# Performance work log

Hardware: AMD Instinct MI355X
Metric: run time of the kernel (lower is better)

## Reference

```python
import jax, jax.numpy as jnp
import numpy as np

LN_EPS = 1e-5
SA_EPS = 1e-8
NUM_ITERS = 3

def layer_norm(x, w, b):
    mu = jnp.mean(x, axis=-1, keepdims=True)
    var = jnp.mean((x - mu) ** 2, axis=-1, keepdims=True)
    return (x - mu) / jnp.sqrt(var + LN_EPS) * w + b


def setup_inputs() -> dict:
    key = jax.random.key(0)
    ks = jax.random.split(key, 24)
    B, C, H, W = 128, 256, 32, 32
    D, S, MH, NC = 64, 8, 128, 15
    s = lambda k, shape, scale=0.02: jax.random.normal(k, shape, dtype=jnp.float32) * scale
    inp = {
        "x1": jax.random.normal(ks[0], (B, C, H, W), dtype=jnp.float32),
        "x2": jax.random.normal(ks[1], (B, C, H, W), dtype=jnp.float32),
        # 1x1 convs stored as [out,in]
        "conv1_w": s(ks[2], (D, C)), "conv1_b": jnp.zeros((D,), jnp.float32),
        "conv2_w": s(ks[3], (D, C)), "conv2_b": jnp.zeros((D,), jnp.float32),
        "norm_w": jnp.ones((D,), jnp.float32), "norm_b": jnp.zeros((D,), jnp.float32),
        "ni_w": jnp.ones((D,), jnp.float32), "ni_b": jnp.zeros((D,), jnp.float32),
        "ns_w": jnp.ones((D,), jnp.float32), "ns_b": jnp.zeros((D,), jnp.float32),
        "nm_w": jnp.ones((D,), jnp.float32), "nm_b": jnp.zeros((D,), jnp.float32),
        "slots_mu": s(ks[4], (1, 1, D), 1.0), "slots_log_sigma": s(ks[5], (1, 1, D), 0.1),
        "Wq": s(ks[6], (D, D), 0.1), "Wk": s(ks[7], (D, D), 0.1), "Wv": s(ks[8], (D, D), 0.1),
        "gru_wih": s(ks[9], (3 * D, D), 0.1), "gru_whh": s(ks[10], (3 * D, D), 0.1),
        "gru_bih": jnp.zeros((3 * D,), jnp.float32), "gru_bhh": jnp.zeros((3 * D,), jnp.float32),
        "mlp_w1": s(ks[11], (MH, D), 0.1), "mlp_b1": jnp.zeros((MH,), jnp.float32),
        "mlp_w2": s(ks[12], (D, MH), 0.1), "mlp_b2": jnp.zeros((D,), jnp.float32),
        "head_w": s(ks[13], (NC, D), 0.1), "head_b": jnp.zeros((NC,), jnp.float32),
        "noise": jax.random.normal(ks[14], (B, S, D), dtype=jnp.float32),
    }
    return inp


def _forward(x1, x2, conv1_w, conv1_b, conv2_w, conv2_b, norm_w, norm_b,
             ni_w, ni_b, ns_w, ns_b, nm_w, nm_b, slots_mu, slots_log_sigma,
             Wq, Wk, Wv, gru_wih, gru_whh, gru_bih, gru_bhh,
             mlp_w1, mlp_b1, mlp_w2, mlp_b2, head_w, head_b, noise):
    B = x1.shape[0]
    D = Wq.shape[0]
    # 1x1 convs then flatten to tokens: [B, H*W, D]
    t1 = jnp.einsum('bchw,dc->bhwd', x1, conv1_w).reshape(B, -1, D) + conv1_b
    t2 = jnp.einsum('bchw,dc->bhwd', x2, conv2_w).reshape(B, -1, D) + conv2_b
    inputs = jnp.concatenate([t1, t2], axis=1)          # [B, N, D]
    inputs = layer_norm(inputs, norm_w, norm_b)

    # SlotAttention
    inputs = layer_norm(inputs, ni_w, ni_b)
    k = inputs @ Wk.T                                    # [B, N, D]
    v = inputs @ Wv.T
    slots = slots_mu + jnp.exp(slots_log_sigma) * noise  # [B, S, D]
    scale = D ** -0.5
    for _ in range(NUM_ITERS):
        slots_prev = slots
        sn = layer_norm(slots, ns_w, ns_b)
        q = (sn @ Wq.T) * scale                          # [B, S, D]
        attn_logits = jnp.einsum('bnd,bsd->bns', k, q)   # [B, N, S]
        attn = jax.nn.softmax(attn_logits, axis=-1) + SA_EPS
        attn = attn / jnp.sum(attn, axis=-2, keepdims=True)
        updates = jnp.einsum('bns,bnd->bsd', attn, v)    # [B, S, D]
        # GRUCell (torch gate order: r, z, n)
        gi = updates @ gru_wih.T + gru_bih               # [B, S, 3D]
        gh = slots_prev @ gru_whh.T + gru_bhh
        ir, iz, inn = jnp.split(gi, 3, axis=-1)
        hr, hz, hn = jnp.split(gh, 3, axis=-1)
        r = jax.nn.sigmoid(ir + hr)
        z = jax.nn.sigmoid(iz + hz)
        n = jnp.tanh(inn + r * hn)
        slots = (1.0 - z) * n + z * slots_prev
        # residual MLP
        h = layer_norm(slots, nm_w, nm_b)
        h = jax.nn.relu(h @ mlp_w1.T + mlp_b1) @ mlp_w2.T + mlp_b2
        slots = slots + h

    fused = jnp.mean(slots, axis=1)                      # [B, D]
    return fused @ head_w.T + head_b                     # [B, n_classes]


def reference(x1, x2, conv1_w, conv1_b, conv2_w, conv2_b, norm_w, norm_b,
              ni_w, ni_b, ns_w, ns_b, nm_w, nm_b, slots_mu, slots_log_sigma,
              Wq, Wk, Wv, gru_wih, gru_whh, gru_bih, gru_bhh,
              mlp_w1, mlp_b1, mlp_w2, mlp_b2, head_w, head_b, noise):
    return _forward(x1, x2, conv1_w, conv1_b, conv2_w, conv2_b, norm_w, norm_b,
                    ni_w, ni_b, ns_w, ns_b, nm_w, nm_b, slots_mu, slots_log_sigma,
                    Wq, Wk, Wv, gru_wih, gru_whh, gru_bih, gru_bhh,
                    mlp_w1, mlp_b1, mlp_w2, mlp_b2, head_w, head_b, noise)
```

## Files before the change

kernel.cpp:

```cpp
#include <hip/hip_runtime.h>
#include <stdint.h>


typedef __bf16 bf16;
typedef __bf16 bf16x8 __attribute__((ext_vector_type(8)));
typedef float  f32x4  __attribute__((ext_vector_type(4)));

#define MFMA16(a, b, c) __builtin_amdgcn_mfma_f32_16x16x32_bf16((a), (b), (c), 0, 0, 0)

__global__ __launch_bounds__(256) void k0_convert(
    const float* __restrict__ c1w, const float* __restrict__ c2w,
    const float* __restrict__ wk,  const float* __restrict__ wvv,
    bf16* __restrict__ wconv, bf16* __restrict__ wkv)
{
  const int i = blockIdx.x * 256 + threadIdx.x;
  if (i < 16384) {
    wconv[i]         = (bf16)c1w[i];
    wconv[16384 + i] = (bf16)c2w[i];
  }
  if (i < 4096) {
    wkv[i]        = (bf16)wk[i];
    wkv[4096 + i] = (bf16)wvv[i];
  }
}

__global__ __launch_bounds__(256) void k1_conv_kv(
    const float* __restrict__ x1, const float* __restrict__ x2,
    const float* __restrict__ c1b, const float* __restrict__ c2b,
    const float* __restrict__ nw,  const float* __restrict__ nb,
    const float* __restrict__ niw, const float* __restrict__ nib,
    const bf16* __restrict__ wconv, const bf16* __restrict__ wkv,
    bf16* __restrict__ kbuf, bf16* __restrict__ vT)
{
  __shared__ union {
    struct { float T[64][65]; bf16 tok[64][72]; } p2;
    struct { float Tk[64][65]; float Tv[64][65]; } kv;
  } U;

  const int bx   = blockIdx.x;
  const int tile = bx & 15;
  const int img  = (bx >> 4) & 1;
  const int b    = bx >> 5;
  const int tid  = threadIdx.x;
  const int lane = tid & 63;
  const int wvid = tid >> 6;
  const int l15  = lane & 15;
  const int quad = lane >> 4;

  const float* xp = (img ? x2 : x1) + (size_t)b * (256 * 1024) + tile * 64;
  const bf16* wc  = wconv + img * (64 * 256);
  const int p     = wvid * 16 + l15;
  const float* xcol = xp + p + (size_t)quad * 8 * 1024;

  float xv[64];
  #pragma unroll
  for (int g = 0; g < 8; ++g)
    #pragma unroll
    for (int j = 0; j < 8; ++j)
      xv[g * 8 + j] = xcol[(size_t)(g * 32 + j) * 1024];

  f32x4 acc[4] = {{0.f,0.f,0.f,0.f},{0.f,0.f,0.f,0.f},{0.f,0.f,0.f,0.f},{0.f,0.f,0.f,0.f}};

  #pragma unroll
  for (int g = 0; g < 8; ++g) {
    bf16x8 af;
    #pragma unroll
    for (int j = 0; j < 8; ++j)
      af[j] = (bf16)xv[g * 8 + j];
    #pragma unroll
    for (int nt = 0; nt < 4; ++nt) {
      const bf16x8 bw = *(const bf16x8*)&wc[(nt * 16 + l15) * 256 + g * 32 + quad * 8];
      acc[nt] = MFMA16(af, bw, acc[nt]);
    }
  }

  {
    const float* cb = img ? c2b : c1b;
    #pragma unroll
    for (int nt = 0; nt < 4; ++nt) {
      const int d = nt * 16 + l15;
      const float bias = cb[d];
      #pragma unroll
      for (int r = 0; r < 4; ++r)
        U.p2.T[wvid * 16 + quad * 4 + r][d] = acc[nt][r] + bias;
    }
  }
  __syncthreads();

  {
    const int pix = tid >> 2, part = tid & 3;
    float xv2[16], yv[16];
    float s = 0.f, s2 = 0.f;
    #pragma unroll
    for (int i = 0; i < 16; ++i) {
      xv2[i] = U.p2.T[pix][part * 16 + i];
      s += xv2[i]; s2 += xv2[i] * xv2[i];
    }
    s  += __shfl_xor(s, 1);  s  += __shfl_xor(s, 2);
    s2 += __shfl_xor(s2, 1); s2 += __shfl_xor(s2, 2);
    float mu   = s * 0.015625f;
    float rstd = rsqrtf(s2 * 0.015625f - mu * mu + 1e-5f);
    s = 0.f; s2 = 0.f;
    #pragma unroll
    for (int i = 0; i < 16; ++i) {
      const int d = part * 16 + i;
      const float y = (xv2[i] - mu) * rstd * nw[d] + nb[d];
      yv[i] = y; s += y; s2 += y * y;
    }
    s  += __shfl_xor(s, 1);  s  += __shfl_xor(s, 2);
    s2 += __shfl_xor(s2, 1); s2 += __shfl_xor(s2, 2);
    mu   = s * 0.015625f;
    rstd = rsqrtf(s2 * 0.015625f - mu * mu + 1e-5f);
    #pragma unroll
    for (int i = 0; i < 16; ++i) {
      const int d = part * 16 + i;
      U.p2.tok[pix][d] = (bf16)((yv[i] - mu) * rstd * niw[d] + nib[d]);
    }
  }
  __syncthreads();

  f32x4 ak[4] = {{0.f,0.f,0.f,0.f},{0.f,0.f,0.f,0.f},{0.f,0.f,0.f,0.f},{0.f,0.f,0.f,0.f}};
  f32x4 av[4] = {{0.f,0.f,0.f,0.f},{0.f,0.f,0.f,0.f},{0.f,0.f,0.f,0.f},{0.f,0.f,0.f,0.f}};
  #pragma unroll
  for (int k0 = 0; k0 < 64; k0 += 32) {
    const bf16x8 af = *(const bf16x8*)&U.p2.tok[wvid * 16 + l15][k0 + quad * 8];
    #pragma unroll
    for (int nt = 0; nt < 4; ++nt) {
      const bf16x8 bk = *(const bf16x8*)&wkv[(nt * 16 + l15) * 64 + k0 + quad * 8];
      const bf16x8 bv = *(const bf16x8*)&wkv[4096 + (nt * 16 + l15) * 64 + k0 + quad * 8];
      ak[nt] = MFMA16(af, bk, ak[nt]);
      av[nt] = MFMA16(af, bv, av[nt]);
    }
  }
  __syncthreads();

  #pragma unroll
  for (int nt = 0; nt < 4; ++nt)
    #pragma unroll
    for (int r = 0; r < 4; ++r) {
      U.kv.Tk[wvid * 16 + quad * 4 + r][nt * 16 + l15] = ak[nt][r];
      U.kv.Tv[nt * 16 + l15][wvid * 16 + quad * 4 + r] = av[nt][r];
    }
  __syncthreads();
  {
    const int row = tid >> 2, dd = (tid & 3) * 16;
    const size_t kb = ((size_t)b * 2048 + img * 1024 + tile * 64) * 64;
    bf16 tb[16];
    #pragma unroll
    for (int i = 0; i < 16; ++i) tb[i] = (bf16)U.kv.Tk[row][dd + i];
    *(bf16x8*)&kbuf[kb + (size_t)row * 64 + dd]     = *(bf16x8*)&tb[0];
    *(bf16x8*)&kbuf[kb + (size_t)row * 64 + dd + 8] = *(bf16x8*)&tb[8];
    #pragma unroll
    for (int i = 0; i < 16; ++i) tb[i] = (bf16)U.kv.Tv[row][dd + i];
    const size_t vb = ((size_t)b * 64 + row) * 2048 + img * 1024 + tile * 64 + dd;
    *(bf16x8*)&vT[vb]     = *(bf16x8*)&tb[0];
    *(bf16x8*)&vT[vb + 8] = *(bf16x8*)&tb[8];
  }
}

__global__ __launch_bounds__(512) void kS0(
    const float* __restrict__ smu, const float* __restrict__ slog,
    const float* __restrict__ noise,
    const float* __restrict__ nsw, const float* __restrict__ nsb,
    const float* __restrict__ Wq,
    float* __restrict__ slotbuf, bf16* __restrict__ qbuf)
{
  __shared__ float tmp[8][66];
  const int b = blockIdx.x, tid = threadIdx.x;
  const int s0 = tid >> 6, d0 = tid & 63;
  const int part = tid & 7, sl = (tid >> 3) & 7, wv = tid >> 6;

  const float sval = smu[d0] + expf(slog[d0]) * noise[((size_t)b * 8 + s0) * 64 + d0];
  slotbuf[((size_t)b * 8 + s0) * 64 + d0] = sval;
  float s = sval, s2 = sval * sval;
  #pragma unroll
  for (int m = 1; m < 64; m <<= 1) { s += __shfl_xor(s, m); s2 += __shfl_xor(s2, m); }
  const float mu = s * 0.015625f;
  const float rstd = rsqrtf(s2 * 0.015625f - mu * mu + 1e-5f);
  tmp[s0][d0] = (sval - mu) * rstd * nsw[d0] + nsb[d0];
  __syncthreads();

  float tm[8];
  #pragma unroll
  for (int i = 0; i < 8; ++i) tm[i] = tmp[sl][part * 8 + i];
  for (int orr = 0; orr < 8; ++orr) {
    const int d = orr * 8 + wv;
    const f32x4 w0 = *(const f32x4*)&Wq[d * 64 + part * 8];
    const f32x4 w1v = *(const f32x4*)&Wq[d * 64 + part * 8 + 4];
    float a = tm[0]*w0[0] + tm[1]*w0[1] + tm[2]*w0[2] + tm[3]*w0[3]
            + tm[4]*w1v[0] + tm[5]*w1v[1] + tm[6]*w1v[2] + tm[7]*w1v[3];
    a += __shfl_xor(a, 1); a += __shfl_xor(a, 2); a += __shfl_xor(a, 4);
    if (part == 0) qbuf[((size_t)b * 8 + sl) * 64 + d] = (bf16)(a * 0.125f);
  }
}

__global__ __launch_bounds__(256) void kA(
    const bf16* __restrict__ kbuf, const bf16* __restrict__ vT,
    const bf16* __restrict__ qbuf,
    float* __restrict__ updpart, float* __restrict__ colpart)
{
  __shared__ bf16  qs[16][72];
  __shared__ bf16  attn_b[16][136];
  __shared__ float updp[4][8][64];
  __shared__ float cspart[4][8];

  const int bx  = blockIdx.x;
  const int b   = bx >> 4, ch = bx & 15;
  const int tid = threadIdx.x;
  const int lane = tid & 63, wvid = tid >> 6;
  const int l15 = lane & 15, quad = lane >> 4;
  const size_t tokbase = (size_t)b * 2048 + ch * 128;

  if (tid < 64) {
    const int s = tid >> 3, o = (tid & 7) * 8;
    *(bf16x8*)&qs[s][o] = *(const bf16x8*)&qbuf[((size_t)b * 8 + s) * 64 + o];
  } else if (tid < 128) {
    const int s = 8 + ((tid - 64) >> 3), o = ((tid - 64) & 7) * 8;
    uint32_t* zp = (uint32_t*)&qs[s][o];
    zp[0] = 0u; zp[1] = 0u; zp[2] = 0u; zp[3] = 0u;
  }
  {
    uint32_t* az = (uint32_t*)&attn_b[8][0];
    for (int i = tid; i < 544; i += 256) az[i] = 0u;
  }
  __syncthreads();

  {
    float cs = 0.f;
    #pragma unroll
    for (int mt = 0; mt < 2; ++mt) {
      const int t0 = wvid * 32 + mt * 16;
      const bf16* kr = kbuf + (tokbase + t0 + l15) * 64 + quad * 8;
      f32x4 lg = {0.f, 0.f, 0.f, 0.f};
      lg = MFMA16(*(const bf16x8*)&kr[0],  *(const bf16x8*)&qs[l15][quad * 8],      lg);
      lg = MFMA16(*(const bf16x8*)&kr[32], *(const bf16x8*)&qs[l15][32 + quad * 8], lg);
      #pragma unroll
      for (int r = 0; r < 4; ++r) {
        const float l = lg[r];
        float m = l;
        m = fmaxf(m, __shfl_xor(m, 1));
        m = fmaxf(m, __shfl_xor(m, 2));
        m = fmaxf(m, __shfl_xor(m, 4));
        const float e = expf(l - m);
        float ss = e;
        ss += __shfl_xor(ss, 1);
        ss += __shfl_xor(ss, 2);
        ss += __shfl_xor(ss, 4);
        const float at = e / ss + 1e-8f;
        if (l15 < 8) {
          const bf16 ab = (bf16)at;
          attn_b[l15][t0 + quad * 4 + r] = ab;
          cs += (float)ab;
        }
      }
    }
    cs += __shfl_xor(cs, 16);
    cs += __shfl_xor(cs, 32);
    if (lane < 8) cspart[wvid][lane] = cs;
  }
  __syncthreads();

  {
    const bf16x8 afr = *(const bf16x8*)&attn_b[l15][wvid * 32 + quad * 8];
    const bf16* vrow = vT + (size_t)b * 131072 + (size_t)ch * 128 + wvid * 32 + quad * 8;
    const f32x4 zero4 = {0.f, 0.f, 0.f, 0.f};
    #pragma unroll
    for (int nt = 0; nt < 4; ++nt) {
      const bf16x8 bv = *(const bf16x8*)&vrow[(size_t)(nt * 16 + l15) * 2048];
      f32x4 dd = MFMA16(afr, bv, zero4);
      if (quad < 2) {
        #pragma unroll
        for (int r = 0; r < 4; ++r)
          updp[wvid][quad * 4 + r][nt * 16 + l15] = dd[r];
      }
    }
  }
  __syncthreads();

  {
    const float* up = &updp[0][0][0];
    float* og = updpart + ((size_t)b * 16 + ch) * 512;
    for (int o = tid; o < 512; o += 256)
      og[o] = up[o] + up[o + 512] + up[o + 1024] + up[o + 1536];
    if (tid < 8)
      colpart[((size_t)b * 16 + ch) * 8 + tid] =
        cspart[0][tid] + cspart[1][tid] + cspart[2][tid] + cspart[3][tid];
  }
}

__global__ __launch_bounds__(512) void kB(
    const float* __restrict__ updpart, const float* __restrict__ colpart,
    float* __restrict__ slotbuf, bf16* __restrict__ qbuf,
    const float* __restrict__ nsw, const float* __restrict__ nsb,
    const float* __restrict__ nmw, const float* __restrict__ nmb,
    const float* __restrict__ Wq,
    const float* __restrict__ wih, const float* __restrict__ whh,
    const float* __restrict__ bih, const float* __restrict__ bhh,
    const float* __restrict__ w1,  const float* __restrict__ b1,
    const float* __restrict__ w2,  const float* __restrict__ b2,
    const float* __restrict__ hwt, const float* __restrict__ hb,
    float* __restrict__ out, const int last)
{
  __shared__ float slots[8][66];
  __shared__ float tmp[8][66];
  __shared__ float gig[8][192], ghg[8][192];
  __shared__ float h1[8][132];
  const int b = blockIdx.x, tid = threadIdx.x;
  const int s0 = tid >> 6, d0 = tid & 63;
  const int part = tid & 7, sl = (tid >> 3) & 7, wv = tid >> 6;

  {
    const float* up = updpart + (size_t)b * 8192 + s0 * 64 + d0;
    float u = 0.f;
    #pragma unroll
    for (int ch = 0; ch < 16; ++ch) u += up[ch * 512];
    const float* cp = colpart + (size_t)b * 128 + s0;
    float cs = 0.f;
    #pragma unroll
    for (int ch = 0; ch < 16; ++ch) cs += cp[ch * 8];
    tmp[s0][d0] = u / cs;
    slots[s0][d0] = slotbuf[((size_t)b * 8 + s0) * 64 + d0];
  }
  __syncthreads();

  {
    float tv[8], sv[8];
    #pragma unroll
    for (int i = 0; i < 8; ++i) { tv[i] = tmp[sl][part * 8 + i]; sv[i] = slots[sl][part * 8 + i]; }
    for (int jr = 0; jr < 24; ++jr) {
      const int j = jr * 8 + wv;
      const f32x4 wa0 = *(const f32x4*)&wih[j * 64 + part * 8];
      const f32x4 wa1 = *(const f32x4*)&wih[j * 64 + part * 8 + 4];
      const f32x4 wb0 = *(const f32x4*)&whh[j * 64 + part * 8];
      const f32x4 wb1 = *(const f32x4*)&whh[j * 64 + part * 8 + 4];
      float a = tv[0]*wa0[0] + tv[1]*wa0[1] + tv[2]*wa0[2] + tv[3]*wa0[3]
              + tv[4]*wa1[0] + tv[5]*wa1[1] + tv[6]*wa1[2] + tv[7]*wa1[3];
      float h = sv[0]*wb0[0] + sv[1]*wb0[1] + sv[2]*wb0[2] + sv[3]*wb0[3]
              + sv[4]*wb1[0] + sv[5]*wb1[1] + sv[6]*wb1[2] + sv[7]*wb1[3];
      a += __shfl_xor(a, 1); a += __shfl_xor(a, 2); a += __shfl_xor(a, 4);
      h += __shfl_xor(h, 1); h += __shfl_xor(h, 2); h += __shfl_xor(h, 4);
      if (part == 0) { gig[sl][j] = a + bih[j]; ghg[sl][j] = h + bhh[j]; }
    }
  }
  __syncthreads();

  float snew;
  {
    const float r  = 1.f / (1.f + expf(-(gig[s0][d0]       + ghg[s0][d0])));
    const float z  = 1.f / (1.f + expf(-(gig[s0][64 + d0]  + ghg[s0][64 + d0])));
    const float nn = tanhf(gig[s0][128 + d0] + r * ghg[s0][128 + d0]);
    snew = (1.f - z) * nn + z * slots[s0][d0];
    slots[s0][d0] = snew;
  }
  {
    float s = snew, s2 = snew * snew;
    #pragma unroll
    for (int m = 1; m < 64; m <<= 1) { s += __shfl_xor(s, m); s2 += __shfl_xor(s2, m); }
    const float mu = s * 0.015625f;
    const float rstd = rsqrtf(s2 * 0.015625f - mu * mu + 1e-5f);
    tmp[s0][d0] = (snew - mu) * rstd * nmw[d0] + nmb[d0];
  }
  __syncthreads();

  {
    float tm[8];
    #pragma unroll
    for (int i = 0; i < 8; ++i) tm[i] = tmp[sl][part * 8 + i];
    for (int jr = 0; jr < 16; ++jr) {
      const int j = jr * 8 + wv;
      const f32x4 w0 = *(const f32x4*)&w1[j * 64 + part * 8];
      const f32x4 w1v = *(const f32x4*)&w1[j * 64 + part * 8 + 4];
      float a = tm[0]*w0[0] + tm[1]*w0[1] + tm[2]*w0[2] + tm[3]*w0[3]
              + tm[4]*w1v[0] + tm[5]*w1v[1] + tm[6]*w1v[2] + tm[7]*w1v[3];
      a += __shfl_xor(a, 1); a += __shfl_xor(a, 2); a += __shfl_xor(a, 4);
      if (part == 0) h1[sl][j] = fmaxf(a + b1[j], 0.f);
    }
  }
  __syncthreads();

  for (int orr = 0; orr < 8; ++orr) {
    const int d = orr * 8 + wv;
    float a = 0.f;
    #pragma unroll
    for (int i = 0; i < 4; ++i) {
      const f32x4 wv4 = *(const f32x4*)&w2[d * 128 + part * 16 + i * 4];
      a += h1[sl][part * 16 + i * 4 + 0] * wv4[0] + h1[sl][part * 16 + i * 4 + 1] * wv4[1]
         + h1[sl][part * 16 + i * 4 + 2] * wv4[2] + h1[sl][part * 16 + i * 4 + 3] * wv4[3];
    }
    a += __shfl_xor(a, 1); a += __shfl_xor(a, 2); a += __shfl_xor(a, 4);
    if (part == 0) slots[sl][d] += a + b2[d];
  }
  __syncthreads();

  const float sfin = slots[s0][d0];
  slotbuf[((size_t)b * 8 + s0) * 64 + d0] = sfin;

  if (!last) {
    float s = sfin, s2 = sfin * sfin;
    #pragma unroll
    for (int m = 1; m < 64; m <<= 1) { s += __shfl_xor(s, m); s2 += __shfl_xor(s2, m); }
    const float mu = s * 0.015625f;
    const float rstd = rsqrtf(s2 * 0.015625f - mu * mu + 1e-5f);
    tmp[s0][d0] = (sfin - mu) * rstd * nsw[d0] + nsb[d0];
    __syncthreads();
    float tm[8];
    #pragma unroll
    for (int i = 0; i < 8; ++i) tm[i] = tmp[sl][part * 8 + i];
    for (int orr = 0; orr < 8; ++orr) {
      const int d = orr * 8 + wv;
      const f32x4 w0 = *(const f32x4*)&Wq[d * 64 + part * 8];
      const f32x4 w1v = *(const f32x4*)&Wq[d * 64 + part * 8 + 4];
      float a = tm[0]*w0[0] + tm[1]*w0[1] + tm[2]*w0[2] + tm[3]*w0[3]
              + tm[4]*w1v[0] + tm[5]*w1v[1] + tm[6]*w1v[2] + tm[7]*w1v[3];
      a += __shfl_xor(a, 1); a += __shfl_xor(a, 2); a += __shfl_xor(a, 4);
      if (part == 0) qbuf[((size_t)b * 8 + sl) * 64 + d] = (bf16)(a * 0.125f);
    }
  } else {
    if (tid < 64) {
      float f = 0.f;
      #pragma unroll
      for (int s = 0; s < 8; ++s) f += slots[s][tid];
      tmp[0][tid] = f * 0.125f;
    }
    __syncthreads();
    if (tid < 15) {
      float a = hb[tid];
      for (int d = 0; d < 64; ++d) a += tmp[0][d] * hwt[tid * 64 + d];
      out[b * 15 + tid] = a;
    }
  }
}

extern "C" void kernel_launch(void* const* d_in, const int* in_sizes, int n_in,
                              void* d_out, int out_size, void* d_ws, size_t ws_size,
                              hipStream_t stream) {
  const float* x1   = (const float*)d_in[0];
  const float* x2   = (const float*)d_in[1];
  const float* c1w  = (const float*)d_in[2];
  const float* c1b  = (const float*)d_in[3];
  const float* c2w  = (const float*)d_in[4];
  const float* c2b  = (const float*)d_in[5];
  const float* nw   = (const float*)d_in[6];
  const float* nb   = (const float*)d_in[7];
  const float* niw  = (const float*)d_in[8];
  const float* nib  = (const float*)d_in[9];
  const float* nsw  = (const float*)d_in[10];
  const float* nsb  = (const float*)d_in[11];
  const float* nmw  = (const float*)d_in[12];
  const float* nmb  = (const float*)d_in[13];
  const float* smu  = (const float*)d_in[14];
  const float* slog = (const float*)d_in[15];
  const float* Wq   = (const float*)d_in[16];
  const float* Wk   = (const float*)d_in[17];
  const float* Wv   = (const float*)d_in[18];
  const float* wih  = (const float*)d_in[19];
  const float* whh  = (const float*)d_in[20];
  const float* bih  = (const float*)d_in[21];
  const float* bhh  = (const float*)d_in[22];
  const float* w1   = (const float*)d_in[23];
  const float* b1   = (const float*)d_in[24];
  const float* w2   = (const float*)d_in[25];
  const float* b2   = (const float*)d_in[26];
  const float* hwt  = (const float*)d_in[27];
  const float* hb   = (const float*)d_in[28];
  const float* noise= (const float*)d_in[29];

  char* ws = (char*)d_ws;
  bf16*  kbuf    = (bf16*)(ws);
  bf16*  vT      = (bf16*)(ws + (size_t)33554432);
  bf16*  wconv   = (bf16*)(ws + (size_t)67108864);
  bf16*  wkv     = (bf16*)(ws + (size_t)67174400);
  float* slotbuf = (float*)(ws + (size_t)67190784);
  bf16*  qbuf    = (bf16*)(ws + (size_t)67452928);
  float* updpart = (float*)(ws + (size_t)67584000);
  float* colpart = (float*)(ws + (size_t)71778304);

  k0_convert<<<dim3(64), dim3(256), 0, stream>>>(c1w, c2w, Wk, Wv, wconv, wkv);
  k1_conv_kv<<<dim3(4096), dim3(256), 0, stream>>>(x1, x2, c1b, c2b, nw, nb, niw, nib,
                                                   wconv, wkv, kbuf, vT);
  kS0<<<dim3(128), dim3(512), 0, stream>>>(smu, slog, noise, nsw, nsb, Wq, slotbuf, qbuf);
  for (int it = 0; it < 3; ++it) {
    kA<<<dim3(2048), dim3(256), 0, stream>>>(kbuf, vT, qbuf, updpart, colpart);
    kB<<<dim3(128), dim3(512), 0, stream>>>(updpart, colpart, slotbuf, qbuf,
                                            nsw, nsb, nmw, nmb, Wq,
                                            wih, whh, bih, bhh, w1, b1, w2, b2,
                                            hwt, hb, (float*)d_out, (it == 2) ? 1 : 0);
  }
}
```

Before: 528.4 us.

## Fuse slot GRU/MLP update into attention kernel, redundantly per chunk block

Each attention block now recomputes the previous iteration's slot update (GRU, MLP, norms, q projection) from double-buffered partial sums, instead of running separate per-batch update kernels. This removes the kS0 and kB launches and the serial 128-block phases between attention passes. Chunks per batch drop from 16 to 8 with 512 threads per block, and a final head kernel applies the last two updates. The cost is the small update math repeated in all 8 blocks of each batch, plus more shared memory per block.

```diff
diff --git a/kernel.cpp b/kernel.cpp
--- a/kernel.cpp
+++ b/kernel.cpp
@@ -158,79 +158,163 @@
   }
 }
 
-__global__ __launch_bounds__(512) void kS0(
+__global__ __launch_bounds__(512) void kA_iter(
+    const bf16* __restrict__ kbuf, const bf16* __restrict__ vT,
     const float* __restrict__ smu, const float* __restrict__ slog,
     const float* __restrict__ noise,
     const float* __restrict__ nsw, const float* __restrict__ nsb,
+    const float* __restrict__ nmw, const float* __restrict__ nmb,
     const float* __restrict__ Wq,
-    float* __restrict__ slotbuf, bf16* __restrict__ qbuf)
+    const float* __restrict__ wih, const float* __restrict__ whh,
+    const float* __restrict__ bih, const float* __restrict__ bhh,
+    const float* __restrict__ w1,  const float* __restrict__ b1,
+    const float* __restrict__ w2,  const float* __restrict__ b2,
+    float* __restrict__ slotbuf, float* __restrict__ updf, float* __restrict__ colf,
+    const int it, const int gin, const int gout)
 {
-  __shared__ float tmp[8][66];
-  const int b = blockIdx.x, tid = threadIdx.x;
-  const int s0 = tid >> 6, d0 = tid & 63;
-  const int part = tid & 7, sl = (tid >> 3) & 7, wv = tid >> 6;
-
-  const float sval = smu[d0] + expf(slog[d0]) * noise[((size_t)b * 8 + s0) * 64 + d0];
-  slotbuf[((size_t)b * 8 + s0) * 64 + d0] = sval;
-  float s = sval, s2 = sval * sval;
-  #pragma unroll
-  for (int m = 1; m < 64; m <<= 1) { s += __shfl_xor(s, m); s2 += __shfl_xor(s2, m); }
-  const float mu = s * 0.015625f;
-  const float rstd = rsqrtf(s2 * 0.015625f - mu * mu + 1e-5f);
-  tmp[s0][d0] = (sval - mu) * rstd * nsw[d0] + nsb[d0];
-  __syncthreads();
-
-  float tm[8];
-  #pragma unroll
-  for (int i = 0; i < 8; ++i) tm[i] = tmp[sl][part * 8 + i];
-  for (int orr = 0; orr < 8; ++orr) {
-    const int d = orr * 8 + wv;
-    const f32x4 w0 = *(const f32x4*)&Wq[d * 64 + part * 8];
-    const f32x4 w1v = *(const f32x4*)&Wq[d * 64 + part * 8 + 4];
-    float a = tm[0]*w0[0] + tm[1]*w0[1] + tm[2]*w0[2] + tm[3]*w0[3]
-            + tm[4]*w1v[0] + tm[5]*w1v[1] + tm[6]*w1v[2] + tm[7]*w1v[3];
-    a += __shfl_xor(a, 1); a += __shfl_xor(a, 2); a += __shfl_xor(a, 4);
-    if (part == 0) qbuf[((size_t)b * 8 + sl) * 64 + d] = (bf16)(a * 0.125f);
-  }
-}
-
-__global__ __launch_bounds__(256) void kA(
-    const bf16* __restrict__ kbuf, const bf16* __restrict__ vT,
-    const bf16* __restrict__ qbuf,
-    float* __restrict__ updpart, float* __restrict__ colpart)
-{
-  __shared__ bf16  qs[16][72];
-  __shared__ bf16  attn_b[16][136];
-  __shared__ float updp[4][8][64];
-  __shared__ float cspart[4][8];
+  __shared__ union {
+    struct { float tmp[8][66]; float slots[8][66];
+             float gig[8][192]; float ghg[8][192]; float h1[8][132]; } P;
+    struct { bf16 attn[16][264]; float updp[8][8][64]; float cspart[8][8]; } A;
+  } U;
+  __shared__ bf16 qs[16][72];
 
   const int bx  = blockIdx.x;
-  const int b   = bx >> 4, ch = bx & 15;
+  const int b   = bx >> 3, ch = bx & 7;
   const int tid = threadIdx.x;
   const int lane = tid & 63, wvid = tid >> 6;
   const int l15 = lane & 15, quad = lane >> 4;
-  const size_t tokbase = (size_t)b * 2048 + ch * 128;
-
-  if (tid < 64) {
-    const int s = tid >> 3, o = (tid & 7) * 8;
-    *(bf16x8*)&qs[s][o] = *(const bf16x8*)&qbuf[((size_t)b * 8 + s) * 64 + o];
-  } else if (tid < 128) {
-    const int s = 8 + ((tid - 64) >> 3), o = ((tid - 64) & 7) * 8;
-    uint32_t* zp = (uint32_t*)&qs[s][o];
-    zp[0] = 0u; zp[1] = 0u; zp[2] = 0u; zp[3] = 0u;
-  }
-  {
-    uint32_t* az = (uint32_t*)&attn_b[8][0];
-    for (int i = tid; i < 544; i += 256) az[i] = 0u;
-  }
-  __syncthreads();
-
-  {
-    float cs = 0.f;
+  const int s0 = tid >> 6, d0 = tid & 63;
+  const int part = tid & 7, sl = (tid >> 3) & 7;
+
+  if (tid < 288) ((uint32_t*)&qs[8][0])[tid] = 0u;
+
+  float snorm;
+  if (it == 1) {
+    snorm = smu[d0] + expf(slog[d0]) * noise[((size_t)b * 8 + s0) * 64 + d0];
+  } else {
+    {
+      const float* up = updf + (((size_t)gin * 128 + b) * 8) * 512 + s0 * 64 + d0;
+      float u = 0.f;
+      #pragma unroll
+      for (int c = 0; c < 8; ++c) u += up[c * 512];
+      const float* cp = colf + (((size_t)gin * 128 + b) * 8) * 8 + s0;
+      float cs = 0.f;
+      #pragma unroll
+      for (int c = 0; c < 8; ++c) cs += cp[c * 8];
+      float sprev;
+      if (it == 2) sprev = smu[d0] + expf(slog[d0]) * noise[((size_t)b * 8 + s0) * 64 + d0];
+      else         sprev = slotbuf[((size_t)b * 8 + s0) * 64 + d0];
+      U.P.tmp[s0][d0]   = u / cs;
+      U.P.slots[s0][d0] = sprev;
+    }
+    __syncthreads();
+
+    {
+      float tv[8], sv[8];
+      #pragma unroll
+      for (int i = 0; i < 8; ++i) { tv[i] = U.P.tmp[sl][part * 8 + i]; sv[i] = U.P.slots[sl][part * 8 + i]; }
+      for (int jr = 0; jr < 24; ++jr) {
+        const int j = jr * 8 + wvid;
+        const f32x4 wa0 = *(const f32x4*)&wih[j * 64 + part * 8];
+        const f32x4 wa1 = *(const f32x4*)&wih[j * 64 + part * 8 + 4];
+        const f32x4 wb0 = *(const f32x4*)&whh[j * 64 + part * 8];
+        const f32x4 wb1 = *(const f32x4*)&whh[j * 64 + part * 8 + 4];
+        float a = tv[0]*wa0[0] + tv[1]*wa0[1] + tv[2]*wa0[2] + tv[3]*wa0[3]
+                + tv[4]*wa1[0] + tv[5]*wa1[1] + tv[6]*wa1[2] + tv[7]*wa1[3];
+        float h = sv[0]*wb0[0] + sv[1]*wb0[1] + sv[2]*wb0[2] + sv[3]*wb0[3]
+                + sv[4]*wb1[0] + sv[5]*wb1[1] + sv[6]*wb1[2] + sv[7]*wb1[3];
+        a += __shfl_xor(a, 1); a += __shfl_xor(a, 2); a += __shfl_xor(a, 4);
+        h += __shfl_xor(h, 1); h += __shfl_xor(h, 2); h += __shfl_xor(h, 4);
+        if (part == 0) { U.P.gig[sl][j] = a + bih[j]; U.P.ghg[sl][j] = h + bhh[j]; }
+      }
+    }
+    __syncthreads();
+
+    {
+      const float rr = 1.f / (1.f + expf(-(U.P.gig[s0][d0]      + U.P.ghg[s0][d0])));
+      const float z  = 1.f / (1.f + expf(-(U.P.gig[s0][64 + d0] + U.P.ghg[s0][64 + d0])));
+      const float nn = tanhf(U.P.gig[s0][128 + d0] + rr * U.P.ghg[s0][128 + d0]);
+      const float snew = (1.f - z) * nn + z * U.P.slots[s0][d0];
+      U.P.slots[s0][d0] = snew;
+      float s = snew, s2 = snew * snew;
+      #pragma unroll
+      for (int m = 1; m < 64; m <<= 1) { s += __shfl_xor(s, m); s2 += __shfl_xor(s2, m); }
+      const float mu = s * 0.015625f;
+      const float rstd = rsqrtf(s2 * 0.015625f - mu * mu + 1e-5f);
+      U.P.tmp[s0][d0] = (snew - mu) * rstd * nmw[d0] + nmb[d0];
+    }
+    __syncthreads();
+
+    {
+      float tm[8];
+      #pragma unroll
+      for (int i = 0; i < 8; ++i) tm[i] = U.P.tmp[sl][part * 8 + i];
+      for (int jr = 0; jr < 16; ++jr) {
+        const int j = jr * 8 + wvid;
+        const f32x4 w0 = *(const f32x4*)&w1[j * 64 + part * 8];
+        const f32x4 w1v = *(const f32x4*)&w1[j * 64 + part * 8 + 4];
+        float a = tm[0]*w0[0] + tm[1]*w0[1] + tm[2]*w0[2] + tm[3]*w0[3]
+                + tm[4]*w1v[0] + tm[5]*w1v[1] + tm[6]*w1v[2] + tm[7]*w1v[3];
+        a += __shfl_xor(a, 1); a += __shfl_xor(a, 2); a += __shfl_xor(a, 4);
+        if (part == 0) U.P.h1[sl][j] = fmaxf(a + b1[j], 0.f);
+      }
+    }
+    __syncthreads();
+
+    for (int orr = 0; orr < 8; ++orr) {
+      const int d = orr * 8 + wvid;
+      float a = 0.f;
+      #pragma unroll
+      for (int i = 0; i < 4; ++i) {
+        const f32x4 wv4 = *(const f32x4*)&w2[d * 128 + part * 16 + i * 4];
+        a += U.P.h1[sl][part * 16 + i * 4 + 0] * wv4[0] + U.P.h1[sl][part * 16 + i * 4 + 1] * wv4[1]
+           + U.P.h1[sl][part * 16 + i * 4 + 2] * wv4[2] + U.P.h1[sl][part * 16 + i * 4 + 3] * wv4[3];
+      }
+      a += __shfl_xor(a, 1); a += __shfl_xor(a, 2); a += __shfl_xor(a, 4);
+      if (part == 0) U.P.slots[sl][d] += a + b2[d];
+    }
+    __syncthreads();
+
+    snorm = U.P.slots[s0][d0];
+    if (it == 2 && ch == 0)
+      slotbuf[((size_t)b * 8 + s0) * 64 + d0] = snorm;
+  }
+
+  {
+    float s = snorm, s2 = snorm * snorm;
+    #pragma unroll
+    for (int m = 1; m < 64; m <<= 1) { s += __shfl_xor(s, m); s2 += __shfl_xor(s2, m); }
+    const float mu = s * 0.015625f;
+    const float rstd = rsqrtf(s2 * 0.015625f - mu * mu + 1e-5f);
+    U.P.tmp[s0][d0] = (snorm - mu) * rstd * nsw[d0] + nsb[d0];
+  }
+  __syncthreads();
+
+  {
+    float tm[8];
+    #pragma unroll
+    for (int i = 0; i < 8; ++i) tm[i] = U.P.tmp[sl][part * 8 + i];
+    for (int orr = 0; orr < 8; ++orr) {
+      const int d = orr * 8 + wvid;
+      const f32x4 w0 = *(const f32x4*)&Wq[d * 64 + part * 8];
+      const f32x4 w1v = *(const f32x4*)&Wq[d * 64 + part * 8 + 4];
+      float a = tm[0]*w0[0] + tm[1]*w0[1] + tm[2]*w0[2] + tm[3]*w0[3]
+              + tm[4]*w1v[0] + tm[5]*w1v[1] + tm[6]*w1v[2] + tm[7]*w1v[3];
+      a += __shfl_xor(a, 1); a += __shfl_xor(a, 2); a += __shfl_xor(a, 4);
+      if (part == 0) qs[sl][d] = (bf16)(a * 0.125f);
+    }
+  }
+  __syncthreads();
+
+  for (int i = tid; i < 1056; i += 512) ((uint32_t*)&U.A.attn[8][0])[i] = 0u;
+
+  {
+    float csacc = 0.f;
+    const size_t tokb = (size_t)b * 2048 + ch * 256 + wvid * 32;
     #pragma unroll
     for (int mt = 0; mt < 2; ++mt) {
-      const int t0 = wvid * 32 + mt * 16;
-      const bf16* kr = kbuf + (tokbase + t0 + l15) * 64 + quad * 8;
+      const bf16* kr = kbuf + (tokb + mt * 16 + l15) * 64 + quad * 8;
       f32x4 lg = {0.f, 0.f, 0.f, 0.f};
       lg = MFMA16(*(const bf16x8*)&kr[0],  *(const bf16x8*)&qs[l15][quad * 8],      lg);
       lg = MFMA16(*(const bf16x8*)&kr[32], *(const bf16x8*)&qs[l15][32 + quad * 8], lg);
@@ -249,20 +333,20 @@
         const float at = e / ss + 1e-8f;
         if (l15 < 8) {
           const bf16 ab = (bf16)at;
-          attn_b[l15][t0 + quad * 4 + r] = ab;
-          cs += (float)ab;
+          U.A.attn[l15][wvid * 32 + mt * 16 + quad * 4 + r] = ab;
+          csacc += (float)ab;
         }
       }
     }
-    cs += __shfl_xor(cs, 16);
-    cs += __shfl_xor(cs, 32);
-    if (lane < 8) cspart[wvid][lane] = cs;
-  }
-  __syncthreads();
-
-  {
-    const bf16x8 afr = *(const bf16x8*)&attn_b[l15][wvid * 32 + quad * 8];
-    const bf16* vrow = vT + (size_t)b * 131072 + (size_t)ch * 128 + wvid * 32 + quad * 8;
+    csacc += __shfl_xor(csacc, 16);
+    csacc += __shfl_xor(csacc, 32);
+    if (lane < 8) U.A.cspart[wvid][lane] = csacc;
+  }
+  __syncthreads();
+
+  {
+    const bf16x8 afr = *(const bf16x8*)&U.A.attn[l15][wvid * 32 + quad * 8];
+    const bf16* vrow = vT + (size_t)b * 131072 + (size_t)ch * 256 + wvid * 32 + quad * 8;
     const f32x4 zero4 = {0.f, 0.f, 0.f, 0.f};
     #pragma unroll
     for (int nt = 0; nt < 4; ++nt) {
@@ -271,35 +355,36 @@
       if (quad < 2) {
         #pragma unroll
         for (int r = 0; r < 4; ++r)
-          updp[wvid][quad * 4 + r][nt * 16 + l15] = dd[r];
-      }
-    }
-  }
-  __syncthreads();
-
-  {
-    const float* up = &updp[0][0][0];
-    float* og = updpart + ((size_t)b * 16 + ch) * 512;
-    for (int o = tid; o < 512; o += 256)
-      og[o] = up[o] + up[o + 512] + up[o + 1024] + up[o + 1536];
-    if (tid < 8)
-      colpart[((size_t)b * 16 + ch) * 8 + tid] =
-        cspart[0][tid] + cspart[1][tid] + cspart[2][tid] + cspart[3][tid];
+          U.A.updp[wvid][quad * 4 + r][nt * 16 + l15] = dd[r];
+      }
+    }
+  }
+  __syncthreads();
+
+  {
+    float u = 0.f;
+    #pragma unroll
+    for (int w = 0; w < 8; ++w) u += U.A.updp[w][s0][d0];
+    updf[(((size_t)gout * 128 + b) * 8 + ch) * 512 + s0 * 64 + d0] = u;
+    if (tid < 8) {
+      float c = 0.f;
+      #pragma unroll
+      for (int w = 0; w < 8; ++w) c += U.A.cspart[w][tid];
+      colf[(((size_t)gout * 128 + b) * 8 + ch) * 8 + tid] = c;
+    }
   }
 }
 
-__global__ __launch_bounds__(512) void kB(
-    const float* __restrict__ updpart, const float* __restrict__ colpart,
-    float* __restrict__ slotbuf, bf16* __restrict__ qbuf,
-    const float* __restrict__ nsw, const float* __restrict__ nsb,
+__global__ __launch_bounds__(512) void kHead(
+    const float* __restrict__ updf, const float* __restrict__ colf,
+    const float* __restrict__ slotbuf,
     const float* __restrict__ nmw, const float* __restrict__ nmb,
-    const float* __restrict__ Wq,
     const float* __restrict__ wih, const float* __restrict__ whh,
     const float* __restrict__ bih, const float* __restrict__ bhh,
     const float* __restrict__ w1,  const float* __restrict__ b1,
     const float* __restrict__ w2,  const float* __restrict__ b2,
     const float* __restrict__ hwt, const float* __restrict__ hb,
-    float* __restrict__ out, const int last)
+    float* __restrict__ out)
 {
   __shared__ float slots[8][66];
   __shared__ float tmp[8][66];
@@ -309,125 +394,101 @@
   const int s0 = tid >> 6, d0 = tid & 63;
   const int part = tid & 7, sl = (tid >> 3) & 7, wv = tid >> 6;
 
-  {
-    const float* up = updpart + (size_t)b * 8192 + s0 * 64 + d0;
-    float u = 0.f;
-    #pragma unroll
-    for (int ch = 0; ch < 16; ++ch) u += up[ch * 512];
-    const float* cp = colpart + (size_t)b * 128 + s0;
-    float cs = 0.f;
-    #pragma unroll
-    for (int ch = 0; ch < 16; ++ch) cs += cp[ch * 8];
-    tmp[s0][d0] = u / cs;
-    slots[s0][d0] = slotbuf[((size_t)b * 8 + s0) * 64 + d0];
-  }
-  __syncthreads();
-
-  {
-    float tv[8], sv[8];
-    #pragma unroll
-    for (int i = 0; i < 8; ++i) { tv[i] = tmp[sl][part * 8 + i]; sv[i] = slots[sl][part * 8 + i]; }
-    for (int jr = 0; jr < 24; ++jr) {
-      const int j = jr * 8 + wv;
-      const f32x4 wa0 = *(const f32x4*)&wih[j * 64 + part * 8];
-      const f32x4 wa1 = *(const f32x4*)&wih[j * 64 + part * 8 + 4];
-      const f32x4 wb0 = *(const f32x4*)&whh[j * 64 + part * 8];
-      const f32x4 wb1 = *(const f32x4*)&whh[j * 64 + part * 8 + 4];
-      float a = tv[0]*wa0[0] + tv[1]*wa0[1] + tv[2]*wa0[2] + tv[3]*wa0[3]
-              + tv[4]*wa1[0] + tv[5]*wa1[1] + tv[6]*wa1[2] + tv[7]*wa1[3];
-      float h = sv[0]*wb0[0] + sv[1]*wb0[1] + sv[2]*wb0[2] + sv[3]*wb0[3]
-              + sv[4]*wb1[0] + sv[5]*wb1[1] + sv[6]*wb1[2] + sv[7]*wb1[3];
-      a += __shfl_xor(a, 1); a += __shfl_xor(a, 2); a += __shfl_xor(a, 4);
-      h += __shfl_xor(h, 1); h += __shfl_xor(h, 2); h += __shfl_xor(h, 4);
-      if (part == 0) { gig[sl][j] = a + bih[j]; ghg[sl][j] = h + bhh[j]; }
-    }
-  }
-  __syncthreads();
-
-  float snew;
-  {
-    const float r  = 1.f / (1.f + expf(-(gig[s0][d0]       + ghg[s0][d0])));
-    const float z  = 1.f / (1.f + expf(-(gig[s0][64 + d0]  + ghg[s0][64 + d0])));
-    const float nn = tanhf(gig[s0][128 + d0] + r * ghg[s0][128 + d0]);
-    snew = (1.f - z) * nn + z * slots[s0][d0];
-    slots[s0][d0] = snew;
-  }
-  {
-    float s = snew, s2 = snew * snew;
-    #pragma unroll
-    for (int m = 1; m < 64; m <<= 1) { s += __shfl_xor(s, m); s2 += __shfl_xor(s2, m); }
-    const float mu = s * 0.015625f;
-    const float rstd = rsqrtf(s2 * 0.015625f - mu * mu + 1e-5f);
-    tmp[s0][d0] = (snew - mu) * rstd * nmw[d0] + nmb[d0];
-  }
-  __syncthreads();
-
-  {
-    float tm[8];
-    #pragma unroll
-    for (int i = 0; i < 8; ++i) tm[i] = tmp[sl][part * 8 + i];
-    for (int jr = 0; jr < 16; ++jr) {
-      const int j = jr * 8 + wv;
-      const f32x4 w0 = *(const f32x4*)&w1[j * 64 + part * 8];
-      const f32x4 w1v = *(const f32x4*)&w1[j * 64 + part * 8 + 4];
-      float a = tm[0]*w0[0] + tm[1]*w0[1] + tm[2]*w0[2] + tm[3]*w0[3]
-              + tm[4]*w1v[0] + tm[5]*w1v[1] + tm[6]*w1v[2] + tm[7]*w1v[3];
-      a += __shfl_xor(a, 1); a += __shfl_xor(a, 2); a += __shfl_xor(a, 4);
-      if (part == 0) h1[sl][j] = fmaxf(a + b1[j], 0.f);
-    }
-  }
-  __syncthreads();
-
-  for (int orr = 0; orr < 8; ++orr) {
-    const int d = orr * 8 + wv;
-    float a = 0.f;
-    #pragma unroll
-    for (int i = 0; i < 4; ++i) {
-      const f32x4 wv4 = *(const f32x4*)&w2[d * 128 + part * 16 + i * 4];
-      a += h1[sl][part * 16 + i * 4 + 0] * wv4[0] + h1[sl][part * 16 + i * 4 + 1] * wv4[1]
-         + h1[sl][part * 16 + i * 4 + 2] * wv4[2] + h1[sl][part * 16 + i * 4 + 3] * wv4[3];
-    }
-    a += __shfl_xor(a, 1); a += __shfl_xor(a, 2); a += __shfl_xor(a, 4);
-    if (part == 0) slots[sl][d] += a + b2[d];
-  }
-  __syncthreads();
-
-  const float sfin = slots[s0][d0];
-  slotbuf[((size_t)b * 8 + s0) * 64 + d0] = sfin;
-
-  if (!last) {
-    float s = sfin, s2 = sfin * sfin;
-    #pragma unroll
-    for (int m = 1; m < 64; m <<= 1) { s += __shfl_xor(s, m); s2 += __shfl_xor(s2, m); }
-    const float mu = s * 0.015625f;
-    const float rstd = rsqrtf(s2 * 0.015625f - mu * mu + 1e-5f);
-    tmp[s0][d0] = (sfin - mu) * rstd * nsw[d0] + nsb[d0];
-    __syncthreads();
-    float tm[8];
-    #pragma unroll
-    for (int i = 0; i < 8; ++i) tm[i] = tmp[sl][part * 8 + i];
+  slots[s0][d0] = slotbuf[((size_t)b * 8 + s0) * 64 + d0];
+
+  for (int pass = 0; pass < 2; ++pass) {
+    const int gin = (pass == 0) ? 1 : 0;
+    {
+      const float* up = updf + (((size_t)gin * 128 + b) * 8) * 512 + s0 * 64 + d0;
+      float u = 0.f;
+      #pragma unroll
+      for (int c = 0; c < 8; ++c) u += up[c * 512];
+      const float* cp = colf + (((size_t)gin * 128 + b) * 8) * 8 + s0;
+      float cs = 0.f;
+      #pragma unroll
+      for (int c = 0; c < 8; ++c) cs += cp[c * 8];
+      tmp[s0][d0] = u / cs;
+    }
+    __syncthreads();
+
+    {
+      float tv[8], sv[8];
+      #pragma unroll
+      for (int i = 0; i < 8; ++i) { tv[i] = tmp[sl][part * 8 + i]; sv[i] = slots[sl][part * 8 + i]; }
+      for (int jr = 0; jr < 24; ++jr) {
+        const int j = jr * 8 + wv;
+        const f32x4 wa0 = *(const f32x4*)&wih[j * 64 + part * 8];
+        const f32x4 wa1 = *(const f32x4*)&wih[j * 64 + part * 8 + 4];
+        const f32x4 wb0 = *(const f32x4*)&whh[j * 64 + part * 8];
+        const f32x4 wb1 = *(const f32x4*)&whh[j * 64 + part * 8 + 4];
+        float a = tv[0]*wa0[0] + tv[1]*wa0[1] + tv[2]*wa0[2] + tv[3]*wa0[3]
+                + tv[4]*wa1[0] + tv[5]*wa1[1] + tv[6]*wa1[2] + tv[7]*wa1[3];
+        float h = sv[0]*wb0[0] + sv[1]*wb0[1] + sv[2]*wb0[2] + sv[3]*wb0[3]
+                + sv[4]*wb1[0] + sv[5]*wb1[1] + sv[6]*wb1[2] + sv[7]*wb1[3];
+        a += __shfl_xor(a, 1); a += __shfl_xor(a, 2); a += __shfl_xor(a, 4);
+        h += __shfl_xor(h, 1); h += __shfl_xor(h, 2); h += __shfl_xor(h, 4);
+        if (part == 0) { gig[sl][j] = a + bih[j]; ghg[sl][j] = h + bhh[j]; }
+      }
+    }
+    __syncthreads();
+
+    {
+      const float rr = 1.f / (1.f + expf(-(gig[s0][d0]      + ghg[s0][d0])));
+      const float z  = 1.f / (1.f + expf(-(gig[s0][64 + d0] + ghg[s0][64 + d0])));
+      const float nn = tanhf(gig[s0][128 + d0] + rr * ghg[s0][128 + d0]);
+      const float snew = (1.f - z) * nn + z * slots[s0][d0];
+      slots[s0][d0] = snew;
+      float s = snew, s2 = snew * snew;
+      #pragma unroll
+      for (int m = 1; m < 64; m <<= 1) { s += __shfl_xor(s, m); s2 += __shfl_xor(s2, m); }
+      const float mu = s * 0.015625f;
+      const float rstd = rsqrtf(s2 * 0.015625f - mu * mu + 1e-5f);
+      tmp[s0][d0] = (snew - mu) * rstd * nmw[d0] + nmb[d0];
+    }
+    __syncthreads();
+
+    {
+      float tm[8];
+      #pragma unroll
+      for (int i = 0; i < 8; ++i) tm[i] = tmp[sl][part * 8 + i];
+      for (int jr = 0; jr < 16; ++jr) {
+        const int j = jr * 8 + wv;
+        const f32x4 w0 = *(const f32x4*)&w1[j * 64 + part * 8];
+        const f32x4 w1v = *(const f32x4*)&w1[j * 64 + part * 8 + 4];
+        float a = tm[0]*w0[0] + tm[1]*w0[1] + tm[2]*w0[2] + tm[3]*w0[3]
+                + tm[4]*w1v[0] + tm[5]*w1v[1] + tm[6]*w1v[2] + tm[7]*w1v[3];
+        a += __shfl_xor(a, 1); a += __shfl_xor(a, 2); a += __shfl_xor(a, 4);
+        if (part == 0) h1[sl][j] = fmaxf(a + b1[j], 0.f);
+      }
+    }
+    __syncthreads();
+
     for (int orr = 0; orr < 8; ++orr) {
       const int d = orr * 8 + wv;
-      const f32x4 w0 = *(const f32x4*)&Wq[d * 64 + part * 8];
-      const f32x4 w1v = *(const f32x4*)&Wq[d * 64 + part * 8 + 4];
-      float a = tm[0]*w0[0] + tm[1]*w0[1] + tm[2]*w0[2] + tm[3]*w0[3]
-              + tm[4]*w1v[0] + tm[5]*w1v[1] + tm[6]*w1v[2] + tm[7]*w1v[3];
+      float a = 0.f;
+      #pragma unroll
+      for (int i = 0; i < 4; ++i) {
+        const f32x4 wv4 = *(const f32x4*)&w2[d * 128 + part * 16 + i * 4];
+        a += h1[sl][part * 16 + i * 4 + 0] * wv4[0] + h1[sl][part * 16 + i * 4 + 1] * wv4[1]
+           + h1[sl][part * 16 + i * 4 + 2] * wv4[2] + h1[sl][part * 16 + i * 4 + 3] * wv4[3];
+      }
       a += __shfl_xor(a, 1); a += __shfl_xor(a, 2); a += __shfl_xor(a, 4);
-      if (part == 0) qbuf[((size_t)b * 8 + sl) * 64 + d] = (bf16)(a * 0.125f);
-    }
-  } else {
-    if (tid < 64) {
-      float f = 0.f;
-      #pragma unroll
-      for (int s = 0; s < 8; ++s) f += slots[s][tid];
-      tmp[0][tid] = f * 0.125f;
-    }
-    __syncthreads();
-    if (tid < 15) {
-      float a = hb[tid];
-      for (int d = 0; d < 64; ++d) a += tmp[0][d] * hwt[tid * 64 + d];
-      out[b * 15 + tid] = a;
-    }
+      if (part == 0) slots[sl][d] += a + b2[d];
+    }
+    __syncthreads();
+  }
+
+  if (tid < 64) {
+    float f = 0.f;
+    #pragma unroll
+    for (int s = 0; s < 8; ++s) f += slots[s][tid];
+    tmp[0][tid] = f * 0.125f;
+  }
+  __syncthreads();
+  if (tid < 15) {
+    float a = hb[tid];
+    for (int d = 0; d < 64; ++d) a += tmp[0][d] * hwt[tid * 64 + d];
+    out[b * 15 + tid] = a;
   }
 }
 
@@ -471,19 +532,25 @@
   bf16*  wconv   = (bf16*)(ws + (size_t)67108864);
   bf16*  wkv     = (bf16*)(ws + (size_t)67174400);
   float* slotbuf = (float*)(ws + (size_t)67190784);
-  bf16*  qbuf    = (bf16*)(ws + (size_t)67452928);
-  float* updpart = (float*)(ws + (size_t)67584000);
-  float* colpart = (float*)(ws + (size_t)71778304);
+  float* updf    = (float*)(ws + (size_t)67452928);
+  float* colf    = (float*)(ws + (size_t)71647232);
 
   k0_convert<<<dim3(64), dim3(256), 0, stream>>>(c1w, c2w, Wk, Wv, wconv, wkv);
   k1_conv_kv<<<dim3(4096), dim3(256), 0, stream>>>(x1, x2, c1b, c2b, nw, nb, niw, nib,
                                                    wconv, wkv, kbuf, vT);
-  kS0<<<dim3(128), dim3(512), 0, stream>>>(smu, slog, noise, nsw, nsb, Wq, slotbuf, qbuf);
-  for (int it = 0; it < 3; ++it) {
-    kA<<<dim3(2048), dim3(256), 0, stream>>>(kbuf, vT, qbuf, updpart, colpart);
-    kB<<<dim3(128), dim3(512), 0, stream>>>(updpart, colpart, slotbuf, qbuf,
-                                            nsw, nsb, nmw, nmb, Wq,
-                                            wih, whh, bih, bhh, w1, b1, w2, b2,
-                                            hwt, hb, (float*)d_out, (it == 2) ? 1 : 0);
-  }
+  kA_iter<<<dim3(1024), dim3(512), 0, stream>>>(kbuf, vT, smu, slog, noise, nsw, nsb,
+                                                nmw, nmb, Wq, wih, whh, bih, bhh,
+                                                w1, b1, w2, b2, slotbuf, updf, colf,
+                                                1, 0, 0);
+  kA_iter<<<dim3(1024), dim3(512), 0, stream>>>(kbuf, vT, smu, slog, noise, nsw, nsb,
+                                                nmw, nmb, Wq, wih, whh, bih, bhh,
+                                                w1, b1, w2, b2, slotbuf, updf, colf,
+                                                2, 0, 1);
+  kA_iter<<<dim3(1024), dim3(512), 0, stream>>>(kbuf, vT, smu, slog, noise, nsw, nsb,
+                                                nmw, nmb, Wq, wih, whh, bih, bhh,
+                                                w1, b1, w2, b2, slotbuf, updf, colf,
+                                                3, 1, 0);
+  kHead<<<dim3(128), dim3(512), 0, stream>>>(updf, colf, slotbuf, nmw, nmb,
+                                             wih, whh, bih, bhh, w1, b1, w2, b2,
+                                             hwt, hb, (float*)d_out);
 }
```

Result: slower. 659.5 us (+24.8%).
